# Optimization experiments

Hardware: AMD Instinct MI355X
Metric: run time of the kernel (lower is better)

The kernel has to match this reference:

```python
import jax, jax.numpy as jnp
import numpy as np

B, IN_DIM, OUT_DIM = 4096, 4096, 4096

def setup_inputs() -> dict:
    key = jax.random.key(0)
    kx, kw, kb = jax.random.split(key, 3)
    x = jax.random.normal(kx, (B, IN_DIM), dtype=jnp.float32)
    W = jax.random.normal(kw, (OUT_DIM, IN_DIM), dtype=jnp.float32) * (1.0 / np.sqrt(IN_DIM))
    b = jax.random.normal(kb, (OUT_DIM,), dtype=jnp.float32) * (1.0 / np.sqrt(IN_DIM))
    return {"x": x, "W": W, "b": b}

def reference(x, W, b):
    # Original computes sum over in_dim of x[:, :, None] * W.T[None, :, :],
    # which is exactly x @ W.T. NOTE: bias is added TWICE in the source
    # (duplicated `out += self.b`), so the faithful output is x @ W.T + 2*b.
    out = jnp.einsum('bi,oi->bo', x, W)  # [B, out_dim]
    out = out + 2.0 * b
    return out
```

## Files before the change

### kernel.cpp

```cpp
#include <hip/hip_runtime.h>
#include <hip/hip_bf16.h>


typedef short bf16x8 __attribute__((ext_vector_type(8)));
typedef short s16x4  __attribute__((ext_vector_type(4)));
typedef short s16x8  __attribute__((ext_vector_type(8)));
typedef float f32x4  __attribute__((ext_vector_type(4)));

constexpr int MDIM = 4096, NDIM = 4096, KDIM = 4096;

typedef const __attribute__((address_space(1))) void* gas_t;
typedef __attribute__((address_space(3))) void*       las_t;

__device__ __forceinline__ short f2bf(float f) {
    __hip_bfloat16 h = __float2bfloat16(f);
    short s; __builtin_memcpy(&s, &h, 2); return s;
}

__global__ __launch_bounds__(256)
void cvt2_f32_bf16(const float* __restrict__ inA, const float* __restrict__ inB,
                   short* __restrict__ outA, short* __restrict__ outB, int n8each) {
    int idx    = blockIdx.x * blockDim.x + threadIdx.x;
    int stride = gridDim.x * blockDim.x;
    for (int i = idx; i < 2 * n8each; i += stride) {
        const f32x4* in4 = (i < n8each) ? (const f32x4*)inA : (const f32x4*)inB;
        s16x8*      out8 = (i < n8each) ? (s16x8*)outA      : (s16x8*)outB;
        int j = (i < n8each) ? i : i - n8each;
        f32x4 a = in4[2 * j];
        f32x4 b = in4[2 * j + 1];
        s16x8 o = { f2bf(a[0]), f2bf(a[1]), f2bf(a[2]), f2bf(a[3]),
                    f2bf(b[0]), f2bf(b[1]), f2bf(b[2]), f2bf(b[3]) };
        out8[j] = o;
    }
}

constexpr int BM = 256, BN = 256, BK = 64;
constexpr int NT  = KDIM / BK;
constexpr int ASZ = BM * BK;
constexpr int BSZ = BN * BK;

template <int Q>
__device__ __forceinline__ void read_aq(const short* base, int rA, int c0, int c1,
                                        bf16x8 (&dst)[2][2]) {
    #pragma unroll
    for (int m = 0; m < 2; ++m) {
        const short* p = &base[(rA + Q * 32 + m * 16) * BK];
        dst[m][0] = *(const bf16x8*)(p + c0);
        dst[m][1] = *(const bf16x8*)(p + c1);
    }
}

template <int Q>
__device__ __forceinline__ void mfma_quad(const bf16x8 (&af)[2][2], const bf16x8 (&bf)[4][2],
                                          f32x4 (&acc)[8][4]) {
    __builtin_amdgcn_s_setprio(1);
    #pragma unroll
    for (int m = 0; m < 2; ++m)
        #pragma unroll
        for (int ni = 0; ni < 4; ++ni)
            #pragma unroll
            for (int kk = 0; kk < 2; ++kk)
                acc[Q * 2 + m][ni] = __builtin_amdgcn_mfma_f32_16x16x32_bf16(
                    af[m][kk], bf[ni][kk], acc[Q * 2 + m][ni], 0, 0, 0);
    __builtin_amdgcn_s_setprio(0);
}

__global__ __launch_bounds__(512, 2)
void gemm_bf16_256(const short* __restrict__ Xb, const short* __restrict__ Wb,
                   const float* __restrict__ Bv, float* __restrict__ Out)
{
    __shared__ short lds[3 * ASZ + 2 * BSZ];

    const int tid  = threadIdx.x;
    const int lane = tid & 63;
    const int wid  = tid >> 6;
    const int wr   = wid >> 2;
    const int wc   = wid & 3;

    const int bid = blockIdx.x;
    const int lin = (bid & 7) * 32 + (bid >> 3);
    const int tm0 = (lin >> 4) * BM;
    const int tn0 = (lin & 15) * BN;

    const int srow = lane >> 3;
    const int sgrn = (lane & 7) ^ srow;
    const char* xbase = (const char*)Xb;
    const char* wbase = (const char*)Wb;
    int aOff[2][2], bOff[2][2], dOff[2][2];
    #pragma unroll
    for (int h = 0; h < 2; ++h) {
        #pragma unroll
        for (int j = 0; j < 2; ++j) {
            const int r = h * 128 + (2 * wid + j) * 8;
            aOff[h][j] = ((tm0 + r + srow) * KDIM + sgrn * 8) * 2;
            bOff[h][j] = ((tn0 + r + srow) * KDIM + sgrn * 8) * 2;
            dOff[h][j] = r * BK;
        }
    }

    const int g   = lane >> 4;
    const int r16 = lane & 15;
    const int c0  = ((0 + g) ^ (r16 & 7)) * 8;
    const int c1  = ((4 + g) ^ (r16 & 7)) * 8;
    const int rA  = wr * 128 + r16;
    const int rB  = wc * 64  + r16;

    f32x4 acc[8][4] = {};
    bf16x8 bf[4][2];
    bf16x8 a0[2][2];

    auto stageA = [&](int kt, int h, short* dst) {
        const size_t kb = (size_t)kt * (BK * 2);
        __builtin_amdgcn_global_load_lds((gas_t)(xbase + kb + aOff[h][0]),
                                         (las_t)(dst + dOff[h][0]), 16, 0, 0);
        __builtin_amdgcn_global_load_lds((gas_t)(xbase + kb + aOff[h][1]),
                                         (las_t)(dst + dOff[h][1]), 16, 0, 0);
    };
    auto stageB = [&](int kt, int h, short* dst) {
        const size_t kb = (size_t)kt * (BK * 2);
        __builtin_amdgcn_global_load_lds((gas_t)(wbase + kb + bOff[h][0]),
                                         (las_t)(dst + dOff[h][0]), 16, 0, 0);
        __builtin_amdgcn_global_load_lds((gas_t)(wbase + kb + bOff[h][1]),
                                         (las_t)(dst + dOff[h][1]), 16, 0, 0);
    };

    short* aSlot0 = (short*)&lds[0];
    short* aSlot1 = (short*)&lds[ASZ];
    short* aSlot2 = (short*)&lds[2 * ASZ];
    short* bSlot0 = (short*)&lds[3 * ASZ];
    short* bSlot1 = (short*)&lds[3 * ASZ + BSZ];

    {
        #pragma unroll
        for (int h = 0; h < 2; ++h) stageB(0, h, bSlot0);
        #pragma unroll
        for (int h = 0; h < 2; ++h) stageA(0, h, aSlot0);
        #pragma unroll
        for (int h = 0; h < 2; ++h) stageB(1, h, bSlot1);
        #pragma unroll
        for (int h = 0; h < 2; ++h) stageA(1, h, aSlot1);
        asm volatile("s_waitcnt vmcnt(8)" ::: "memory");
        asm volatile("s_barrier" ::: "memory");
        #pragma unroll
        for (int ni = 0; ni < 4; ++ni) {
            const short* p = &bSlot0[(rB + ni * 16) * BK];
            bf[ni][0] = *(const bf16x8*)(p + c0);
            bf[ni][1] = *(const bf16x8*)(p + c1);
        }
        read_aq<0>(aSlot0, rA, c0, c1, a0);
    }

    short* aCur = aSlot0; short* aNxt = aSlot1; short* aStg = aSlot2;
    short* bCur = bSlot0; short* bNxt = bSlot1;

    for (int t = 0; t < NT; ++t) {
        bf16x8 aq1[2][2];
        read_aq<1>(aCur, rA, c0, c1, aq1);
        if (t + 2 < NT) { stageA(t + 2, 0, aStg); stageA(t + 2, 1, aStg); }
        mfma_quad<0>(a0, bf, acc);

        bf16x8 aq2[2][2];
        read_aq<2>(aCur, rA, c0, c1, aq2);
        if (t + 2 < NT) stageB(t + 2, 0, bCur);
        mfma_quad<1>(aq1, bf, acc);

        bf16x8 aq3[2][2];
        read_aq<3>(aCur, rA, c0, c1, aq3);
        if (t + 2 < NT) stageB(t + 2, 1, bCur);
        if (t < NT - 2) { asm volatile("s_waitcnt vmcnt(8)" ::: "memory"); }
        else            { asm volatile("s_waitcnt vmcnt(0)" ::: "memory"); }
        asm volatile("s_barrier" ::: "memory");
        mfma_quad<2>(aq2, bf, acc);

        __builtin_amdgcn_s_setprio(1);
        #pragma unroll
        for (int ni = 0; ni < 4; ++ni) {
            #pragma unroll
            for (int kk = 0; kk < 2; ++kk) {
                const int cc = kk ? c1 : c0;
                acc[6][ni] = __builtin_amdgcn_mfma_f32_16x16x32_bf16(
                                 aq3[0][kk], bf[ni][kk], acc[6][ni], 0, 0, 0);
                acc[7][ni] = __builtin_amdgcn_mfma_f32_16x16x32_bf16(
                                 aq3[1][kk], bf[ni][kk], acc[7][ni], 0, 0, 0);
                if (t + 1 < NT)
                    bf[ni][kk] = *(const bf16x8*)(&bNxt[(rB + ni * 16) * BK] + cc);
            }
        }
        __builtin_amdgcn_s_setprio(0);
        if (t + 1 < NT) read_aq<0>(aNxt, rA, c0, c1, a0);
        asm volatile("s_barrier" ::: "memory");

        short* tmp = aCur; aCur = aNxt; aNxt = aStg; aStg = tmp;
        tmp = bCur; bCur = bNxt; bNxt = tmp;
    }

    float bb[4];
    #pragma unroll
    for (int ni = 0; ni < 4; ++ni)
        bb[ni] = 2.0f * Bv[tn0 + wc * 64 + ni * 16 + r16];

    #pragma unroll
    for (int mi = 0; mi < 8; ++mi) {
        #pragma unroll
        for (int r = 0; r < 4; ++r) {
            const int row = tm0 + wr * 128 + mi * 16 + g * 4 + r;
            float* orow = Out + (size_t)row * NDIM + tn0 + wc * 64 + r16;
            #pragma unroll
            for (int ni = 0; ni < 4; ++ni)
                orow[ni * 16] = acc[mi][ni][r] + bb[ni];
        }
    }
}

constexpr int FBM = 128, FBN = 128, FBK = 32, LDT = FBK + 8;
__global__ __launch_bounds__(256)
void gemm_xwt_bias2(const float* __restrict__ X, const float* __restrict__ W,
                    const float* __restrict__ Bv, float* __restrict__ Out)
{
    __shared__ short As[FBM * LDT];
    __shared__ short Bs[FBN * LDT];
    const int tid  = threadIdx.x;
    const int lane = tid & 63;
    const int wid  = tid >> 6;
    const int wr   = wid >> 1;
    const int wc   = wid & 1;
    const int tm0  = blockIdx.y * FBM;
    const int tn0  = blockIdx.x * FBN;
    const int srow = tid >> 3;
    const int scol = (tid & 7) * 4;
    const int g    = lane >> 4;
    const int r16  = lane & 15;
    f32x4 acc[4][4] = {};
    const float* xg = X + (size_t)(tm0 + srow) * KDIM + scol;
    const float* wg = W + (size_t)(tn0 + srow) * KDIM + scol;
    for (int k0 = 0; k0 < KDIM; k0 += FBK) {
        #pragma unroll
        for (int i = 0; i < 4; ++i) {
            const int row = srow + 32 * i;
            f32x4 av = *(const f32x4*)(xg + (size_t)(32 * i) * KDIM + k0);
            f32x4 bv = *(const f32x4*)(wg + (size_t)(32 * i) * KDIM + k0);
            s16x4 pa = { f2bf(av[0]), f2bf(av[1]), f2bf(av[2]), f2bf(av[3]) };
            s16x4 pb = { f2bf(bv[0]), f2bf(bv[1]), f2bf(bv[2]), f2bf(bv[3]) };
            *(s16x4*)&As[row * LDT + scol] = pa;
            *(s16x4*)&Bs[row * LDT + scol] = pb;
        }
        __syncthreads();
        bf16x8 af[4], bfr[4];
        #pragma unroll
        for (int mi = 0; mi < 4; ++mi)
            af[mi] = *(const bf16x8*)&As[(wr * 64 + mi * 16 + r16) * LDT + g * 8];
        #pragma unroll
        for (int ni = 0; ni < 4; ++ni)
            bfr[ni] = *(const bf16x8*)&Bs[(wc * 64 + ni * 16 + r16) * LDT + g * 8];
        #pragma unroll
        for (int mi = 0; mi < 4; ++mi)
            #pragma unroll
            for (int ni = 0; ni < 4; ++ni)
                acc[mi][ni] = __builtin_amdgcn_mfma_f32_16x16x32_bf16(
                                  af[mi], bfr[ni], acc[mi][ni], 0, 0, 0);
        __syncthreads();
    }
    float bb[4];
    #pragma unroll
    for (int ni = 0; ni < 4; ++ni)
        bb[ni] = 2.0f * Bv[tn0 + wc * 64 + ni * 16 + r16];
    #pragma unroll
    for (int mi = 0; mi < 4; ++mi)
        #pragma unroll
        for (int r = 0; r < 4; ++r) {
            const int row = tm0 + wr * 64 + mi * 16 + g * 4 + r;
            float* orow = Out + (size_t)row * NDIM + tn0 + wc * 64 + r16;
            #pragma unroll
            for (int ni = 0; ni < 4; ++ni)
                orow[ni * 16] = acc[mi][ni][r] + bb[ni];
        }
}

extern "C" void kernel_launch(void* const* d_in, const int* in_sizes, int n_in,
                              void* d_out, int out_size, void* d_ws, size_t ws_size,
                              hipStream_t stream) {
    const float* X  = (const float*)d_in[0];
    const float* W  = (const float*)d_in[1];
    const float* Bv = (const float*)d_in[2];
    float* Out = (float*)d_out;

    const size_t nElem = (size_t)MDIM * KDIM;
    const size_t need  = 2 * nElem * sizeof(short);

    if (ws_size >= need) {
        short* Xb = (short*)d_ws;
        short* Wb = Xb + nElem;
        const int n8 = (int)(nElem / 8);
        cvt2_f32_bf16<<<4096, 256, 0, stream>>>(X, W, Xb, Wb, n8);
        gemm_bf16_256<<<dim3(256), 512, 0, stream>>>(Xb, Wb, Bv, Out);
    } else {
        dim3 grid(NDIM / FBN, MDIM / FBM);
        gemm_xwt_bias2<<<grid, 256, 0, stream>>>(X, W, Bv, Out);
    }
}
```

Measured before the change: 135.5 us.

## Switch GEMM inner loop to 32x32x16 MFMA with matching LDS swizzle

Replaces the 16x16x32 bf16 MFMA tiling with 32x32x16 MFMA instructions. Each wave now holds 4x2 f32x16 accumulators instead of 8x4 f32x4. The LDS swizzle on the staging writes and the fragment reads is changed to fit the 32-row access pattern, and the epilogue index math is updated for the 32x32 output layout. The larger MFMA cuts the instruction count and the number of LDS fragment reads per FLOP, at the cost of a new swizzle that must stay free of bank conflicts and still be correct.

```diff
diff --git a/kernel.cpp b/kernel.cpp
--- a/kernel.cpp
+++ b/kernel.cpp
@@ -6,6 +6,7 @@
 typedef short s16x4  __attribute__((ext_vector_type(4)));
 typedef short s16x8  __attribute__((ext_vector_type(8)));
 typedef float f32x4  __attribute__((ext_vector_type(4)));
+typedef float f32x16 __attribute__((ext_vector_type(16)));
 
 constexpr int MDIM = 4096, NDIM = 4096, KDIM = 4096;
 
@@ -39,29 +40,25 @@
 constexpr int ASZ = BM * BK;
 constexpr int BSZ = BN * BK;
 
-template <int Q>
-__device__ __forceinline__ void read_aq(const short* base, int rA, int c0, int c1,
-                                        bf16x8 (&dst)[2][2]) {
-    #pragma unroll
-    for (int m = 0; m < 2; ++m) {
-        const short* p = &base[(rA + Q * 32 + m * 16) * BK];
-        dst[m][0] = *(const bf16x8*)(p + c0);
-        dst[m][1] = *(const bf16x8*)(p + c1);
-    }
-}
-
-template <int Q>
-__device__ __forceinline__ void mfma_quad(const bf16x8 (&af)[2][2], const bf16x8 (&bf)[4][2],
-                                          f32x4 (&acc)[8][4]) {
+template <int MF>
+__device__ __forceinline__ void read_a32(const short* base, int rA32, int g2,
+                                         const int (&fz)[4], bf16x8 (&dst)[4]) {
+    const short* p = &base[(rA32 + MF * 32) * BK];
+    #pragma unroll
+    for (int ks = 0; ks < 4; ++ks)
+        dst[ks] = *(const bf16x8*)(p + ((2 * ks + g2) ^ fz[MF]) * 8);
+}
+
+template <int MF>
+__device__ __forceinline__ void mfma_q32(const bf16x8 (&af)[4], const bf16x8 (&bf)[2][4],
+                                         f32x16 (&acc)[4][2]) {
     __builtin_amdgcn_s_setprio(1);
     #pragma unroll
-    for (int m = 0; m < 2; ++m)
-        #pragma unroll
-        for (int ni = 0; ni < 4; ++ni)
-            #pragma unroll
-            for (int kk = 0; kk < 2; ++kk)
-                acc[Q * 2 + m][ni] = __builtin_amdgcn_mfma_f32_16x16x32_bf16(
-                    af[m][kk], bf[ni][kk], acc[Q * 2 + m][ni], 0, 0, 0);
+    for (int ks = 0; ks < 4; ++ks)
+        #pragma unroll
+        for (int nf = 0; nf < 2; ++nf)
+            acc[MF][nf] = __builtin_amdgcn_mfma_f32_32x32x16_bf16(
+                af[ks], bf[nf][ks], acc[MF][nf], 0, 0, 0);
     __builtin_amdgcn_s_setprio(0);
 }
 
@@ -83,7 +80,6 @@
     const int tn0 = (lin & 15) * BN;
 
     const int srow = lane >> 3;
-    const int sgrn = (lane & 7) ^ srow;
     const char* xbase = (const char*)Xb;
     const char* wbase = (const char*)Wb;
     int aOff[2][2], bOff[2][2], dOff[2][2];
@@ -91,23 +87,26 @@
     for (int h = 0; h < 2; ++h) {
         #pragma unroll
         for (int j = 0; j < 2; ++j) {
-            const int r = h * 128 + (2 * wid + j) * 8;
-            aOff[h][j] = ((tm0 + r + srow) * KDIM + sgrn * 8) * 2;
-            bOff[h][j] = ((tn0 + r + srow) * KDIM + sgrn * 8) * 2;
+            const int r  = h * 128 + (2 * wid + j) * 8;
+            const int sg = (lane & 7) ^ srow ^ ((2 * wid + j) & 7);
+            aOff[h][j] = ((tm0 + r + srow) * KDIM + sg * 8) * 2;
+            bOff[h][j] = ((tn0 + r + srow) * KDIM + sg * 8) * 2;
             dOff[h][j] = r * BK;
         }
     }
 
-    const int g   = lane >> 4;
-    const int r16 = lane & 15;
-    const int c0  = ((0 + g) ^ (r16 & 7)) * 8;
-    const int c1  = ((4 + g) ^ (r16 & 7)) * 8;
-    const int rA  = wr * 128 + r16;
-    const int rB  = wc * 64  + r16;
-
-    f32x4 acc[8][4] = {};
-    bf16x8 bf[4][2];
-    bf16x8 a0[2][2];
+    const int l31 = lane & 31;
+    const int g2  = lane >> 5;
+    int fz[4];
+    #pragma unroll
+    for (int q = 0; q < 4; ++q)
+        fz[q] = (l31 & 7) ^ ((q * 4 + (l31 >> 3)) & 7);
+    const int rA32 = wr * 128 + l31;
+    const int rB32 = wc * 64  + l31;
+
+    f32x16 acc[4][2] = {};
+    bf16x8 bf[2][4];
+    bf16x8 a0[4];
 
     auto stageA = [&](int kt, int h, short* dst) {
         const size_t kb = (size_t)kt * (BK * 2);
@@ -142,72 +141,70 @@
         asm volatile("s_waitcnt vmcnt(8)" ::: "memory");
         asm volatile("s_barrier" ::: "memory");
         #pragma unroll
-        for (int ni = 0; ni < 4; ++ni) {
-            const short* p = &bSlot0[(rB + ni * 16) * BK];
-            bf[ni][0] = *(const bf16x8*)(p + c0);
-            bf[ni][1] = *(const bf16x8*)(p + c1);
-        }
-        read_aq<0>(aSlot0, rA, c0, c1, a0);
+        for (int ks = 0; ks < 4; ++ks) {
+            bf[0][ks] = *(const bf16x8*)(&bSlot0[(rB32)      * BK] + ((2 * ks + g2) ^ fz[0]) * 8);
+            bf[1][ks] = *(const bf16x8*)(&bSlot0[(rB32 + 32) * BK] + ((2 * ks + g2) ^ fz[1]) * 8);
+        }
+        read_a32<0>(aSlot0, rA32, g2, fz, a0);
     }
 
     short* aCur = aSlot0; short* aNxt = aSlot1; short* aStg = aSlot2;
     short* bCur = bSlot0; short* bNxt = bSlot1;
 
     for (int t = 0; t < NT; ++t) {
-        bf16x8 aq1[2][2];
-        read_aq<1>(aCur, rA, c0, c1, aq1);
+        bf16x8 aq1[4];
+        read_a32<1>(aCur, rA32, g2, fz, aq1);
         if (t + 2 < NT) { stageA(t + 2, 0, aStg); stageA(t + 2, 1, aStg); }
-        mfma_quad<0>(a0, bf, acc);
-
-        bf16x8 aq2[2][2];
-        read_aq<2>(aCur, rA, c0, c1, aq2);
+        mfma_q32<0>(a0, bf, acc);
+
+        bf16x8 aq2[4];
+        read_a32<2>(aCur, rA32, g2, fz, aq2);
         if (t + 2 < NT) stageB(t + 2, 0, bCur);
-        mfma_quad<1>(aq1, bf, acc);
-
-        bf16x8 aq3[2][2];
-        read_aq<3>(aCur, rA, c0, c1, aq3);
+        mfma_q32<1>(aq1, bf, acc);
+
+        bf16x8 aq3[4];
+        read_a32<3>(aCur, rA32, g2, fz, aq3);
         if (t + 2 < NT) stageB(t + 2, 1, bCur);
         if (t < NT - 2) { asm volatile("s_waitcnt vmcnt(8)" ::: "memory"); }
         else            { asm volatile("s_waitcnt vmcnt(0)" ::: "memory"); }
         asm volatile("s_barrier" ::: "memory");
-        mfma_quad<2>(aq2, bf, acc);
+        mfma_q32<2>(aq2, bf, acc);
 
         __builtin_amdgcn_s_setprio(1);
         #pragma unroll
-        for (int ni = 0; ni < 4; ++ni) {
-            #pragma unroll
-            for (int kk = 0; kk < 2; ++kk) {
-                const int cc = kk ? c1 : c0;
-                acc[6][ni] = __builtin_amdgcn_mfma_f32_16x16x32_bf16(
-                                 aq3[0][kk], bf[ni][kk], acc[6][ni], 0, 0, 0);
-                acc[7][ni] = __builtin_amdgcn_mfma_f32_16x16x32_bf16(
-                                 aq3[1][kk], bf[ni][kk], acc[7][ni], 0, 0, 0);
-                if (t + 1 < NT)
-                    bf[ni][kk] = *(const bf16x8*)(&bNxt[(rB + ni * 16) * BK] + cc);
+        for (int ks = 0; ks < 4; ++ks) {
+            acc[3][0] = __builtin_amdgcn_mfma_f32_32x32x16_bf16(
+                            aq3[ks], bf[0][ks], acc[3][0], 0, 0, 0);
+            acc[3][1] = __builtin_amdgcn_mfma_f32_32x32x16_bf16(
+                            aq3[ks], bf[1][ks], acc[3][1], 0, 0, 0);
+            if (t + 1 < NT) {
+                bf[0][ks] = *(const bf16x8*)(&bNxt[(rB32)      * BK] + ((2 * ks + g2) ^ fz[0]) * 8);
+                bf[1][ks] = *(const bf16x8*)(&bNxt[(rB32 + 32) * BK] + ((2 * ks + g2) ^ fz[1]) * 8);
             }
         }
         __builtin_amdgcn_s_setprio(0);
-        if (t + 1 < NT) read_aq<0>(aNxt, rA, c0, c1, a0);
+        if (t + 1 < NT) read_a32<0>(aNxt, rA32, g2, fz, a0);
         asm volatile("s_barrier" ::: "memory");
 
         short* tmp = aCur; aCur = aNxt; aNxt = aStg; aStg = tmp;
         tmp = bCur; bCur = bNxt; bNxt = tmp;
     }
 
-    float bb[4];
-    #pragma unroll
-    for (int ni = 0; ni < 4; ++ni)
-        bb[ni] = 2.0f * Bv[tn0 + wc * 64 + ni * 16 + r16];
-
-    #pragma unroll
-    for (int mi = 0; mi < 8; ++mi) {
-        #pragma unroll
-        for (int r = 0; r < 4; ++r) {
-            const int row = tm0 + wr * 128 + mi * 16 + g * 4 + r;
-            float* orow = Out + (size_t)row * NDIM + tn0 + wc * 64 + r16;
+    float bb[2];
+    #pragma unroll
+    for (int nf = 0; nf < 2; ++nf)
+        bb[nf] = 2.0f * Bv[tn0 + wc * 64 + nf * 32 + l31];
+
+    #pragma unroll
+    for (int mf = 0; mf < 4; ++mf) {
+        #pragma unroll
+        for (int reg = 0; reg < 16; ++reg) {
+            const int row = tm0 + wr * 128 + mf * 32
+                          + (reg & 3) + 8 * (reg >> 2) + 4 * g2;
+            float* orow = Out + (size_t)row * NDIM + tn0 + wc * 64 + l31;
             #pragma unroll
-            for (int ni = 0; ni < 4; ++ni)
-                orow[ni * 16] = acc[mi][ni][r] + bb[ni];
+            for (int nf = 0; nf < 2; ++nf)
+                orow[nf * 32] = acc[mf][nf][reg] + bb[nf];
         }
     }
 }
```

Measured after the change: 150.3 us. 10.9% more time.

## Use 4 waves with 128x128 per-wave tiles in bf16 GEMM

Applied to the files above, without the earlier changes.

Restructures the 256x256 block GEMM from 8 waves (each 128x64) to 4 waves (each 128x128), doubling per-wave accumulators to 8x8 MFMA tiles so each LDS-loaded B fragment is reused across more A rows. The pipeline is reorganized into eight row-wise MFMA groups with interleaved global-to-LDS staging, and the vmcnt waits are adjusted. This cuts LDS read traffic per MFMA and barrier participants, but it roughly doubles VGPR pressure (256 accumulator floats per lane) and halves the wave count per block, which reduces latency hiding.

```diff
diff --git a/kernel.cpp b/kernel.cpp
--- a/kernel.cpp
+++ b/kernel.cpp
@@ -39,33 +39,27 @@
 constexpr int ASZ = BM * BK;
 constexpr int BSZ = BN * BK;
 
-template <int Q>
-__device__ __forceinline__ void read_aq(const short* base, int rA, int c0, int c1,
-                                        bf16x8 (&dst)[2][2]) {
-    #pragma unroll
-    for (int m = 0; m < 2; ++m) {
-        const short* p = &base[(rA + Q * 32 + m * 16) * BK];
-        dst[m][0] = *(const bf16x8*)(p + c0);
-        dst[m][1] = *(const bf16x8*)(p + c1);
-    }
-}
-
-template <int Q>
-__device__ __forceinline__ void mfma_quad(const bf16x8 (&af)[2][2], const bf16x8 (&bf)[4][2],
-                                          f32x4 (&acc)[8][4]) {
+__device__ __forceinline__ void read_am(const short* base, int row, int c0, int c1,
+                                        bf16x8 (&dst)[2]) {
+    const short* p = &base[row * BK];
+    dst[0] = *(const bf16x8*)(p + c0);
+    dst[1] = *(const bf16x8*)(p + c1);
+}
+
+template <int M>
+__device__ __forceinline__ void mfma_row(const bf16x8 (&af)[2], const bf16x8 (&bf)[8][2],
+                                         f32x4 (&acc)[8][8]) {
     __builtin_amdgcn_s_setprio(1);
     #pragma unroll
-    for (int m = 0; m < 2; ++m)
-        #pragma unroll
-        for (int ni = 0; ni < 4; ++ni)
-            #pragma unroll
-            for (int kk = 0; kk < 2; ++kk)
-                acc[Q * 2 + m][ni] = __builtin_amdgcn_mfma_f32_16x16x32_bf16(
-                    af[m][kk], bf[ni][kk], acc[Q * 2 + m][ni], 0, 0, 0);
+    for (int ni = 0; ni < 8; ++ni)
+        #pragma unroll
+        for (int kk = 0; kk < 2; ++kk)
+            acc[M][ni] = __builtin_amdgcn_mfma_f32_16x16x32_bf16(
+                af[kk], bf[ni][kk], acc[M][ni], 0, 0, 0);
     __builtin_amdgcn_s_setprio(0);
 }
 
-__global__ __launch_bounds__(512, 2)
+__global__ __launch_bounds__(256, 1)
 void gemm_bf16_256(const short* __restrict__ Xb, const short* __restrict__ Wb,
                    const float* __restrict__ Bv, float* __restrict__ Out)
 {
@@ -74,8 +68,8 @@
     const int tid  = threadIdx.x;
     const int lane = tid & 63;
     const int wid  = tid >> 6;
-    const int wr   = wid >> 2;
-    const int wc   = wid & 3;
+    const int wr   = wid >> 1;
+    const int wc   = wid & 1;
 
     const int bid = blockIdx.x;
     const int lin = (bid & 7) * 32 + (bid >> 3);
@@ -86,16 +80,13 @@
     const int sgrn = (lane & 7) ^ srow;
     const char* xbase = (const char*)Xb;
     const char* wbase = (const char*)Wb;
-    int aOff[2][2], bOff[2][2], dOff[2][2];
-    #pragma unroll
-    for (int h = 0; h < 2; ++h) {
-        #pragma unroll
-        for (int j = 0; j < 2; ++j) {
-            const int r = h * 128 + (2 * wid + j) * 8;
-            aOff[h][j] = ((tm0 + r + srow) * KDIM + sgrn * 8) * 2;
-            bOff[h][j] = ((tn0 + r + srow) * KDIM + sgrn * 8) * 2;
-            dOff[h][j] = r * BK;
-        }
+    int aOff[8], bOff[8], dOff[8];
+    #pragma unroll
+    for (int j = 0; j < 8; ++j) {
+        const int r = 64 * wid + 8 * j;
+        aOff[j] = ((tm0 + r + srow) * KDIM + sgrn * 8) * 2;
+        bOff[j] = ((tn0 + r + srow) * KDIM + sgrn * 8) * 2;
+        dOff[j] = r * BK;
     }
 
     const int g   = lane >> 4;
@@ -103,25 +94,21 @@
     const int c0  = ((0 + g) ^ (r16 & 7)) * 8;
     const int c1  = ((4 + g) ^ (r16 & 7)) * 8;
     const int rA  = wr * 128 + r16;
-    const int rB  = wc * 64  + r16;
-
-    f32x4 acc[8][4] = {};
-    bf16x8 bf[4][2];
-    bf16x8 a0[2][2];
-
-    auto stageA = [&](int kt, int h, short* dst) {
+    const int rB  = wc * 128 + r16;
+
+    f32x4 acc[8][8] = {};
+    bf16x8 bf[8][2];
+    bf16x8 a0[2];
+
+    auto stageA = [&](int kt, int j, short* dst) {
         const size_t kb = (size_t)kt * (BK * 2);
-        __builtin_amdgcn_global_load_lds((gas_t)(xbase + kb + aOff[h][0]),
-                                         (las_t)(dst + dOff[h][0]), 16, 0, 0);
-        __builtin_amdgcn_global_load_lds((gas_t)(xbase + kb + aOff[h][1]),
-                                         (las_t)(dst + dOff[h][1]), 16, 0, 0);
+        __builtin_amdgcn_global_load_lds((gas_t)(xbase + kb + aOff[j]),
+                                         (las_t)(dst + dOff[j]), 16, 0, 0);
     };
-    auto stageB = [&](int kt, int h, short* dst) {
+    auto stageB = [&](int kt, int j, short* dst) {
         const size_t kb = (size_t)kt * (BK * 2);
-        __builtin_amdgcn_global_load_lds((gas_t)(wbase + kb + bOff[h][0]),
-                                         (las_t)(dst + dOff[h][0]), 16, 0, 0);
-        __builtin_amdgcn_global_load_lds((gas_t)(wbase + kb + bOff[h][1]),
-                                         (las_t)(dst + dOff[h][1]), 16, 0, 0);
+        __builtin_amdgcn_global_load_lds((gas_t)(wbase + kb + bOff[j]),
+                                         (las_t)(dst + dOff[j]), 16, 0, 0);
     };
 
     short* aSlot0 = (short*)&lds[0];
@@ -132,81 +119,90 @@
 
     {
         #pragma unroll
-        for (int h = 0; h < 2; ++h) stageB(0, h, bSlot0);
-        #pragma unroll
-        for (int h = 0; h < 2; ++h) stageA(0, h, aSlot0);
-        #pragma unroll
-        for (int h = 0; h < 2; ++h) stageB(1, h, bSlot1);
-        #pragma unroll
-        for (int h = 0; h < 2; ++h) stageA(1, h, aSlot1);
-        asm volatile("s_waitcnt vmcnt(8)" ::: "memory");
+        for (int j = 0; j < 8; ++j) stageB(0, j, bSlot0);
+        #pragma unroll
+        for (int j = 0; j < 8; ++j) stageA(0, j, aSlot0);
+        #pragma unroll
+        for (int j = 0; j < 8; ++j) stageB(1, j, bSlot1);
+        #pragma unroll
+        for (int j = 0; j < 8; ++j) stageA(1, j, aSlot1);
+        asm volatile("s_waitcnt vmcnt(16)" ::: "memory");
         asm volatile("s_barrier" ::: "memory");
         #pragma unroll
-        for (int ni = 0; ni < 4; ++ni) {
+        for (int ni = 0; ni < 8; ++ni) {
             const short* p = &bSlot0[(rB + ni * 16) * BK];
             bf[ni][0] = *(const bf16x8*)(p + c0);
             bf[ni][1] = *(const bf16x8*)(p + c1);
         }
-        read_aq<0>(aSlot0, rA, c0, c1, a0);
+        read_am(aSlot0, rA, c0, c1, a0);
     }
 
     short* aCur = aSlot0; short* aNxt = aSlot1; short* aStg = aSlot2;
     short* bCur = bSlot0; short* bNxt = bSlot1;
 
     for (int t = 0; t < NT; ++t) {
-        bf16x8 aq1[2][2];
-        read_aq<1>(aCur, rA, c0, c1, aq1);
-        if (t + 2 < NT) { stageA(t + 2, 0, aStg); stageA(t + 2, 1, aStg); }
-        mfma_quad<0>(a0, bf, acc);
-
-        bf16x8 aq2[2][2];
-        read_aq<2>(aCur, rA, c0, c1, aq2);
-        if (t + 2 < NT) stageB(t + 2, 0, bCur);
-        mfma_quad<1>(aq1, bf, acc);
-
-        bf16x8 aq3[2][2];
-        read_aq<3>(aCur, rA, c0, c1, aq3);
-        if (t + 2 < NT) stageB(t + 2, 1, bCur);
-        if (t < NT - 2) { asm volatile("s_waitcnt vmcnt(8)" ::: "memory"); }
+        const bool sA = (t + 2 < NT);
+        bf16x8 amE[2], amO[2];
+
+        read_am(aCur, rA + 16, c0, c1, amO);
+        if (sA) { stageA(t + 2, 0, aStg); stageA(t + 2, 1, aStg); }
+        mfma_row<0>(a0, bf, acc);
+        read_am(aCur, rA + 32, c0, c1, amE);
+        if (sA) { stageA(t + 2, 2, aStg); stageA(t + 2, 3, aStg); }
+        mfma_row<1>(amO, bf, acc);
+        read_am(aCur, rA + 48, c0, c1, amO);
+        if (sA) { stageA(t + 2, 4, aStg); stageA(t + 2, 5, aStg); }
+        mfma_row<2>(amE, bf, acc);
+        read_am(aCur, rA + 64, c0, c1, amE);
+        if (sA) { stageA(t + 2, 6, aStg); stageA(t + 2, 7, aStg); }
+        mfma_row<3>(amO, bf, acc);
+        read_am(aCur, rA + 80, c0, c1, amO);
+        if (sA) { stageB(t + 2, 0, bCur); stageB(t + 2, 1, bCur); }
+        mfma_row<4>(amE, bf, acc);
+        read_am(aCur, rA + 96, c0, c1, amE);
+        if (sA) { stageB(t + 2, 2, bCur); stageB(t + 2, 3, bCur); }
+        mfma_row<5>(amO, bf, acc);
+        read_am(aCur, rA + 112, c0, c1, amO);
+        if (sA) { stageB(t + 2, 4, bCur); stageB(t + 2, 5, bCur); }
+        if (t < NT - 2) { asm volatile("s_waitcnt vmcnt(14)" ::: "memory"); }
         else            { asm volatile("s_waitcnt vmcnt(0)" ::: "memory"); }
         asm volatile("s_barrier" ::: "memory");
-        mfma_quad<2>(aq2, bf, acc);
+        mfma_row<6>(amE, bf, acc);
 
         __builtin_amdgcn_s_setprio(1);
         #pragma unroll
-        for (int ni = 0; ni < 4; ++ni) {
+        for (int ni = 0; ni < 8; ++ni) {
             #pragma unroll
             for (int kk = 0; kk < 2; ++kk) {
                 const int cc = kk ? c1 : c0;
-                acc[6][ni] = __builtin_amdgcn_mfma_f32_16x16x32_bf16(
-                                 aq3[0][kk], bf[ni][kk], acc[6][ni], 0, 0, 0);
                 acc[7][ni] = __builtin_amdgcn_mfma_f32_16x16x32_bf16(
-                                 aq3[1][kk], bf[ni][kk], acc[7][ni], 0, 0, 0);
+                                 amO[kk], bf[ni][kk], acc[7][ni], 0, 0, 0);
                 if (t + 1 < NT)
                     bf[ni][kk] = *(const bf16x8*)(&bNxt[(rB + ni * 16) * BK] + cc);
             }
         }
         __builtin_amdgcn_s_setprio(0);
-        if (t + 1 < NT) read_aq<0>(aNxt, rA, c0, c1, a0);
+        if (t + 1 < NT) read_am(aNxt, rA, c0, c1, a0);
+        if (sA) { stageB(t + 2, 6, bCur); stageB(t + 2, 7, bCur); }
         asm volatile("s_barrier" ::: "memory");
 
         short* tmp = aCur; aCur = aNxt; aNxt = aStg; aStg = tmp;
         tmp = bCur; bCur = bNxt; bNxt = tmp;
     }
 
-    float bb[4];
-    #pragma unroll
-    for (int ni = 0; ni < 4; ++ni)
-        bb[ni] = 2.0f * Bv[tn0 + wc * 64 + ni * 16 + r16];
+    float bb[8];
+    #pragma unroll
+    for (int ni = 0; ni < 8; ++ni)
+        bb[ni] = 2.0f * Bv[tn0 + wc * 128 + ni * 16 + r16];
 
     #pragma unroll
     for (int mi = 0; mi < 8; ++mi) {
         #pragma unroll
         for (int r = 0; r < 4; ++r) {
             const int row = tm0 + wr * 128 + mi * 16 + g * 4 + r;
-            float* orow = Out + (size_t)row * NDIM + tn0 + wc * 64 + r16;
-            #pragma unroll
-            for (int ni = 0; ni < 4; ++ni)
+            float* orow = Out + (size_t)row * NDIM + tn0 + wc * 128 + r16;
+            #pragma unroll
+            for (int ni = 0; ni < 8; ++ni)
                 orow[ni * 16] = acc[mi][ni][r] + bb[ni];
         }
     }
@@ -292,7 +288,7 @@
         short* Wb = Xb + nElem;
         const int n8 = (int)(nElem / 8);
         cvt2_f32_bf16<<<4096, 256, 0, stream>>>(X, W, Xb, Wb, n8);
-        gemm_bf16_256<<<dim3(256), 512, 0, stream>>>(Xb, Wb, Bv, Out);
+        gemm_bf16_256<<<dim3(256), 256, 0, stream>>>(Xb, Wb, Bv, Out);
     } else {
         dim3 grid(NDIM / FBN, MDIM / FBM);
         gemm_xwt_bias2<<<grid, 256, 0, stream>>>(X, W, Bv, Out);
```

Result: no change. 137.9 us (+1.8%).
